# Performance work log

Hardware: AMD Instinct MI355X
Metric: run time of the kernel (lower is better)

The kernel has to match this reference:

```python
import jax, jax.numpy as jnp
import numpy as np

NEG_SLOPE = 0.2


def gat_layer(x, src, dst, W, att_src, att_dst, bias, concat):
    # x: [N, Fin]; W: [Fin, H*C]; att_*: [H, C]; bias: [H*C] or [C]
    n = x.shape[0]
    H, C = att_src.shape
    h = (x @ W).reshape(n, H, C)                      # [N,H,C]
    a_src = jnp.einsum('nhc,hc->nh', h, att_src)      # [N,H]
    a_dst = jnp.einsum('nhc,hc->nh', h, att_dst)      # [N,H]
    e = a_src[src] + a_dst[dst]                       # [E,H]
    e = jnp.where(e > 0, e, NEG_SLOPE * e)            # leaky_relu(0.2)
    # segment softmax over edges grouped by destination node
    m = jax.ops.segment_max(e, dst, num_segments=n)   # [N,H]
    m = jnp.where(jnp.isfinite(m), m, 0.0)            # empty segments
    ex = jnp.exp(e - m[dst])                          # [E,H]
    s = jax.ops.segment_sum(ex, dst, num_segments=n)  # [N,H]
    alpha = ex / (s[dst] + 1e-16)                     # [E,H]
    msg = h[src] * alpha[..., None]                   # [E,H,C]
    out = jax.ops.segment_sum(msg, dst, num_segments=n)  # [N,H,C]
    out = out.reshape(n, H * C) if concat else out.mean(axis=1)
    return out + bias


def setup_inputs() -> dict:
    key = jax.random.key(0)
    ks = jax.random.split(key, 10)
    N, E, FIN, HID, HEADS, OUT = 50000, 800000, 128, 64, 4, 16
    x = jax.random.normal(ks[0], (N, FIN), dtype=jnp.float32)
    edge_index = jax.random.randint(ks[1], (2, E), 0, N, dtype=jnp.int32)
    sc = 0.05
    return {
        'x': x,
        'edge_index': edge_index,
        'W1': jax.random.normal(ks[2], (FIN, HEADS * HID), jnp.float32) * sc,
        'att_src1': jax.random.normal(ks[3], (HEADS, HID), jnp.float32) * sc,
        'att_dst1': jax.random.normal(ks[4], (HEADS, HID), jnp.float32) * sc,
        'b1': jnp.zeros((HEADS * HID,), jnp.float32),
        'W2': jax.random.normal(ks[5], (HEADS * HID, OUT), jnp.float32) * sc,
        'att_src2': jax.random.normal(ks[6], (1, OUT), jnp.float32) * sc,
        'att_dst2': jax.random.normal(ks[7], (1, OUT), jnp.float32) * sc,
        'b2': jnp.zeros((OUT,), jnp.float32),
    }


def reference(x, edge_index, W1, att_src1, att_dst1, b1, W2, att_src2, att_dst2, b2):
    src, dst = edge_index[0], edge_index[1]
    h = gat_layer(x, src, dst, W1, att_src1, att_dst1, b1, concat=True)
    h = jax.nn.relu(h)
    # dropout is identity in eval mode
    out = gat_layer(h, src, dst, W2, att_src2, att_dst2, b2, concat=False)
    return out
```

## Files before the change

### kernel.cpp

```cpp
#include <hip/hip_runtime.h>
#include <hip/hip_bf16.h>

#define FIN 128
#define HC 256
#define H1 4
#define C1 64
#define OUT2 16

typedef __attribute__((ext_vector_type(8))) short bf16x8;
typedef __attribute__((ext_vector_type(4))) float f32x4;

__device__ inline float bf2f(unsigned short u) {
    union { unsigned int i; float f; } v; v.i = ((unsigned int)u) << 16; return v.f;
}
__device__ inline unsigned short f2bf(float f) {
    union { float f; unsigned int i; } v; v.f = f;
    unsigned int i = v.i;
    return (unsigned short)((i + 0x7FFFu + ((i >> 16) & 1u)) >> 16);
}
__device__ inline unsigned int pack2(float a, float b) {
    return (unsigned int)f2bf(a) | ((unsigned int)f2bf(b) << 16);
}

__global__ __launch_bounds__(256) void prep_kernel(
    const float* __restrict__ W1, unsigned short* __restrict__ W1t,
    const int* __restrict__ dst, int* __restrict__ counts, int E)
{
    int b = blockIdx.x;
    if (b < 128) {
        int t = b * 256 + threadIdx.x;
        int c = t >> 7, k = t & 127;
        W1t[t] = f2bf(W1[k * HC + c]);
    } else {
        int e = (b - 128) * 256 + threadIdx.x;
        if (e < E) atomicAdd(&counts[dst[e]], 1);
    }
}

__global__ __launch_bounds__(256) void gemm1_mfma_kernel(
    const float* __restrict__ x, const unsigned short* __restrict__ W1t,
    const float* __restrict__ att_src, const float* __restrict__ att_dst,
    unsigned short* __restrict__ h1, float* __restrict__ a_src,
    float* __restrict__ a_dst, int N)
{
    const int t  = threadIdx.x;
    const int wv = t >> 6;
    const int l  = t & 63;
    const int c0 = l & 15;
    const int h  = l >> 4;
    const int R0 = blockIdx.x * 64 + wv * 16;

    f32x4 acc[16];
    #pragma unroll
    for (int j = 0; j < 16; j++) acc[j] = (f32x4){0.f, 0.f, 0.f, 0.f};

    int arow = R0 + c0;
    if (arow > N - 1) arow = N - 1;
    const float* xrow = x + (size_t)arow * FIN;

    for (int kb = 0; kb < FIN; kb += 32) {
        float4 f0 = *(const float4*)&xrow[kb + 8 * h];
        float4 f1 = *(const float4*)&xrow[kb + 8 * h + 4];
        union { bf16x8 v; unsigned int u[4]; } af;
        af.u[0] = pack2(f0.x, f0.y);
        af.u[1] = pack2(f0.z, f0.w);
        af.u[2] = pack2(f1.x, f1.y);
        af.u[3] = pack2(f1.z, f1.w);
        #pragma unroll
        for (int j = 0; j < 16; j++) {
            int col = 16 * j + c0;
            union { bf16x8 v; uint4 u; } bf;
            bf.u = *(const uint4*)&W1t[(size_t)col * FIN + kb + 8 * h];
            acc[j] = __builtin_amdgcn_mfma_f32_16x16x32_bf16(af.v, bf.v, acc[j], 0, 0, 0);
        }
    }

    float avs[16], avd[16];
    #pragma unroll
    for (int j = 0; j < 16; j++) {
        avs[j] = att_src[16 * j + c0];
        avd[j] = att_dst[16 * j + c0];
    }
    f32x4 ps[4], pd[4];
    #pragma unroll
    for (int hd = 0; hd < 4; hd++) {
        ps[hd] = (f32x4){0.f, 0.f, 0.f, 0.f};
        pd[hd] = (f32x4){0.f, 0.f, 0.f, 0.f};
        #pragma unroll
        for (int jj = 0; jj < 4; jj++) {
            int j = 4 * hd + jj;
            #pragma unroll
            for (int r = 0; r < 4; r++) {
                ps[hd][r] = fmaf(acc[j][r], avs[j], ps[hd][r]);
                pd[hd][r] = fmaf(acc[j][r], avd[j], pd[hd][r]);
            }
        }
    }
    #pragma unroll
    for (int hd = 0; hd < 4; hd++)
        #pragma unroll
        for (int r = 0; r < 4; r++) {
            float s = ps[hd][r], d = pd[hd][r];
            s += __shfl_xor(s, 1, 64);  d += __shfl_xor(d, 1, 64);
            s += __shfl_xor(s, 2, 64);  d += __shfl_xor(d, 2, 64);
            s += __shfl_xor(s, 4, 64);  d += __shfl_xor(d, 4, 64);
            s += __shfl_xor(s, 8, 64);  d += __shfl_xor(d, 8, 64);
            ps[hd][r] = s;  pd[hd][r] = d;
        }
    {
        float s_sel = 0.f, d_sel = 0.f;
        #pragma unroll
        for (int hd = 0; hd < 4; hd++)
            #pragma unroll
            for (int r = 0; r < 4; r++) {
                bool m = (c0 == hd * 4 + r);
                s_sel = m ? ps[hd][r] : s_sel;
                d_sel = m ? pd[hd][r] : d_sel;
            }
        int row = R0 + 4 * h + (c0 & 3);
        if (row < N) {
            a_src[row * 4 + (c0 >> 2)] = s_sel;
            a_dst[row * 4 + (c0 >> 2)] = d_sel;
        }
    }

    #pragma unroll
    for (int r = 0; r < 4; r++) {
        int row = R0 + 4 * h + r;
        if (row < N) {
            unsigned short* hp = &h1[(size_t)row * HC + c0];
            #pragma unroll
            for (int j = 0; j < 16; j++)
                hp[16 * j] = f2bf(acc[j][r]);
        }
    }
}

__global__ __launch_bounds__(1024) void scan1_kernel(
    const int* __restrict__ counts, int* __restrict__ rowptr,
    int* __restrict__ bsum, int n)
{
    __shared__ int sm[1024];
    int tid = threadIdx.x;
    int i = blockIdx.x * 1024 + tid;
    int v = (i < n) ? counts[i] : 0;
    sm[tid] = v;
    __syncthreads();
    for (int off = 1; off < 1024; off <<= 1) {
        int tv = (tid >= off) ? sm[tid - off] : 0;
        __syncthreads();
        sm[tid] += tv;
        __syncthreads();
    }
    if (i < n) rowptr[i] = sm[tid] - v;
    if (tid == 1023) bsum[blockIdx.x] = sm[1023];
}

__global__ __launch_bounds__(1024) void scan2_kernel(
    int* __restrict__ bsum, int nb)
{
    __shared__ int sm[1024];
    int tid = threadIdx.x;
    int v = (tid < nb) ? bsum[tid] : 0;
    sm[tid] = v;
    __syncthreads();
    for (int off = 1; off < 1024; off <<= 1) {
        int tv = (tid >= off) ? sm[tid - off] : 0;
        __syncthreads();
        sm[tid] += tv;
        __syncthreads();
    }
    if (tid < nb) bsum[tid] = sm[tid] - v;
}

__global__ __launch_bounds__(256) void scatter_kernel(
    const int* __restrict__ src, const int* __restrict__ dst,
    const int* __restrict__ rowptr, const int* __restrict__ bsum,
    int* __restrict__ cursor,
    const float* __restrict__ a_src, const float* __restrict__ a_dst,
    uint4* __restrict__ csr_rec, int E)
{
    int e = blockIdx.x * blockDim.x + threadIdx.x;
    if (e >= E) return;
    int s = src[e], d = dst[e];
    int pos = rowptr[d] + bsum[d >> 10] + atomicAdd(&cursor[d], 1);
    float4 av = *(const float4*)&a_src[(size_t)s * 4];
    float4 bv = *(const float4*)&a_dst[(size_t)d * 4];
    float w0, w1, w2, w3, v;
    v = av.x + bv.x; v = v > 0.f ? v : 0.2f * v; w0 = __expf(v);
    v = av.y + bv.y; v = v > 0.f ? v : 0.2f * v; w1 = __expf(v);
    v = av.z + bv.z; v = v > 0.f ? v : 0.2f * v; w2 = __expf(v);
    v = av.w + bv.w; v = v > 0.f ? v : 0.2f * v; w3 = __expf(v);
    uint4 rec;
    rec.x = (unsigned int)s;
    rec.y = (unsigned int)d;
    rec.z = pack2(w0, w1);
    rec.w = pack2(w2, w3);
    csr_rec[pos] = rec;
}

__global__ __launch_bounds__(256) void agg1_kernel(
    const unsigned short* __restrict__ h1,
    const uint4* __restrict__ csr_rec, const int* __restrict__ rowptr,
    const int* __restrict__ bsum,
    const float* __restrict__ b1, const float* __restrict__ W2,
    const float* __restrict__ att_src2, const float* __restrict__ att_dst2,
    float* __restrict__ h2, float* __restrict__ a_src2, float* __restrict__ a_dst2,
    int N, int E)
{
    __shared__ float o_sh[4][272];
    int wave = (int)((blockIdx.x * blockDim.x + threadIdx.x) >> 6);
    if (wave >= N) return;
    int node = __builtin_amdgcn_readfirstlane(wave);
    int wv = (threadIdx.x >> 6);
    int l = threadIdx.x & 63;
    int h = l >> 4;
    int rs = rowptr[node] + bsum[node >> 10];
    int re = (node + 1 == N) ? E : rowptr[node + 1] + bsum[(node + 1) >> 10];
    float a0 = 0.f, a1 = 0.f, a2 = 0.f, a3 = 0.f, sw = 0.f;
    int p = rs;
    for (; p + 8 <= re; p += 8) {
        uint4 r[8];
        #pragma unroll
        for (int j = 0; j < 8; j++) r[j] = csr_rec[p + j];
        uint2 hv[8];
        #pragma unroll
        for (int j = 0; j < 8; j++)
            hv[j] = *(const uint2*)&h1[(size_t)(int)r[j].x * HC + 4 * l];
        #pragma unroll
        for (int j = 0; j < 8; j++) {
            unsigned int wsel = (h & 2) ? r[j].w : r[j].z;
            float wv_ = bf2f((unsigned short)((h & 1) ? (wsel >> 16) : (wsel & 0xffff)));
            a0 = fmaf(wv_, bf2f((unsigned short)(hv[j].x & 0xffff)), a0);
            a1 = fmaf(wv_, bf2f((unsigned short)(hv[j].x >> 16)), a1);
            a2 = fmaf(wv_, bf2f((unsigned short)(hv[j].y & 0xffff)), a2);
            a3 = fmaf(wv_, bf2f((unsigned short)(hv[j].y >> 16)), a3);
            sw += wv_;
        }
    }
    for (; p < re; p++) {
        uint4 r = csr_rec[p];
        uint2 hv = *(const uint2*)&h1[(size_t)(int)r.x * HC + 4 * l];
        unsigned int wsel = (h & 2) ? r.w : r.z;
        float wv_ = bf2f((unsigned short)((h & 1) ? (wsel >> 16) : (wsel & 0xffff)));
        a0 = fmaf(wv_, bf2f((unsigned short)(hv.x & 0xffff)), a0);
        a1 = fmaf(wv_, bf2f((unsigned short)(hv.x >> 16)), a1);
        a2 = fmaf(wv_, bf2f((unsigned short)(hv.y & 0xffff)), a2);
        a3 = fmaf(wv_, bf2f((unsigned short)(hv.y >> 16)), a3);
        sw += wv_;
    }
    float inv = 1.f / (sw + 1e-16f);
    float4 bv = *(const float4*)&b1[4 * l];
    float o0 = fmaxf(a0 * inv + bv.x, 0.f);
    float o1 = fmaxf(a1 * inv + bv.y, 0.f);
    float o2 = fmaxf(a2 * inv + bv.z, 0.f);
    float o3 = fmaxf(a3 * inv + bv.w, 0.f);

    float* my = o_sh[wv];
    *(float4*)&my[4 * l + 4 * h] = make_float4(o0, o1, o2, o3);
    asm volatile("s_waitcnt lgkmcnt(0)" ::: "memory");
    __builtin_amdgcn_sched_barrier(0);
    int q = h;
    int c = l & 15;
    float part = 0.f;
    #pragma unroll
    for (int m = 0; m < 16; m++) {
        float4 ov = *(const float4*)&my[68 * q + 4 * m];
        const float* w = &W2[(size_t)(64 * q + 4 * m) * OUT2 + c];
        part = fmaf(ov.x, w[0],  part);
        part = fmaf(ov.y, w[16], part);
        part = fmaf(ov.z, w[32], part);
        part = fmaf(ov.w, w[48], part);
    }
    part += __shfl_xor(part, 16, 64);
    part += __shfl_xor(part, 32, 64);
    float ps = part * att_src2[c];
    float pdv = part * att_dst2[c];
    ps += __shfl_xor(ps, 1, 64);  pdv += __shfl_xor(pdv, 1, 64);
    ps += __shfl_xor(ps, 2, 64);  pdv += __shfl_xor(pdv, 2, 64);
    ps += __shfl_xor(ps, 4, 64);  pdv += __shfl_xor(pdv, 4, 64);
    ps += __shfl_xor(ps, 8, 64);  pdv += __shfl_xor(pdv, 8, 64);
    if (l == 0) { a_src2[node] = ps; a_dst2[node] = pdv; }
    if (l < 16) h2[(size_t)node * OUT2 + l] = part;
}

__global__ __launch_bounds__(256) void agg2_kernel(
    const float* __restrict__ h2,
    const int* __restrict__ csr_rec_i,
    const float* __restrict__ a_src2, const float* __restrict__ a_dst2,
    const int* __restrict__ rowptr, const int* __restrict__ bsum,
    const float* __restrict__ b2, float* __restrict__ out, int N, int E)
{
    int wave = (int)((blockIdx.x * blockDim.x + threadIdx.x) >> 6);
    if (wave >= N) return;
    int node = __builtin_amdgcn_readfirstlane(wave);
    int l = threadIdx.x & 63;
    int g = l >> 4, c = l & 15;
    int rs = rowptr[node] + bsum[node >> 10];
    int re = (node + 1 == N) ? E : rowptr[node + 1] + bsum[(node + 1) >> 10];
    float ad = a_dst2[node];
    float acc = 0.f, sw = 0.f;
    int p = rs + g;
    for (; p + 12 < re; p += 16) {
        int sn0 = csr_rec_i[(size_t)(p     ) * 4];
        int sn1 = csr_rec_i[(size_t)(p +  4) * 4];
        int sn2 = csr_rec_i[(size_t)(p +  8) * 4];
        int sn3 = csr_rec_i[(size_t)(p + 12) * 4];
        float e0 = a_src2[sn0] + ad;
        float e1 = a_src2[sn1] + ad;
        float e2 = a_src2[sn2] + ad;
        float e3 = a_src2[sn3] + ad;
        float x0 = h2[(size_t)sn0 * OUT2 + c];
        float x1 = h2[(size_t)sn1 * OUT2 + c];
        float x2 = h2[(size_t)sn2 * OUT2 + c];
        float x3 = h2[(size_t)sn3 * OUT2 + c];
        e0 = e0 > 0.f ? e0 : 0.2f * e0;
        e1 = e1 > 0.f ? e1 : 0.2f * e1;
        e2 = e2 > 0.f ? e2 : 0.2f * e2;
        e3 = e3 > 0.f ? e3 : 0.2f * e3;
        float w0 = __expf(e0), w1 = __expf(e1), w2 = __expf(e2), w3 = __expf(e3);
        acc = fmaf(w0, x0, acc);
        acc = fmaf(w1, x1, acc);
        acc = fmaf(w2, x2, acc);
        acc = fmaf(w3, x3, acc);
        sw += (w0 + w1) + (w2 + w3);
    }
    for (; p < re; p += 4) {
        int sn = csr_rec_i[(size_t)p * 4];
        float e0 = a_src2[sn] + ad;
        e0 = e0 > 0.f ? e0 : 0.2f * e0;
        float w0 = __expf(e0);
        acc = fmaf(w0, h2[(size_t)sn * OUT2 + c], acc);
        sw += w0;
    }
    acc += __shfl_xor(acc, 16, 64);
    acc += __shfl_xor(acc, 32, 64);
    sw += __shfl_xor(sw, 16, 64);
    sw += __shfl_xor(sw, 32, 64);
    if (l < 16)
        out[(size_t)node * OUT2 + l] = acc / (sw + 1e-16f) + b2[l];
}

extern "C" void kernel_launch(void* const* d_in, const int* in_sizes, int n_in,
                              void* d_out, int out_size, void* d_ws, size_t ws_size,
                              hipStream_t stream)
{
    const float* x        = (const float*)d_in[0];
    const int*   ei       = (const int*)d_in[1];
    const float* W1       = (const float*)d_in[2];
    const float* att_src1 = (const float*)d_in[3];
    const float* att_dst1 = (const float*)d_in[4];
    const float* b1       = (const float*)d_in[5];
    const float* W2       = (const float*)d_in[6];
    const float* att_src2 = (const float*)d_in[7];
    const float* att_dst2 = (const float*)d_in[8];
    const float* b2       = (const float*)d_in[9];
    float* out = (float*)d_out;

    const int N = in_sizes[0] / FIN;
    const int E = in_sizes[1] / 2;
    const int* srcv = ei;
    const int* dstv = ei + E;

    char* base = (char*)d_ws;
    #define ALLOC(ptr, type, nelem) \
        type* ptr = (type*)base; base += (((size_t)(nelem) * sizeof(type) + 255) & ~(size_t)255);
    ALLOC(h1,      unsigned short, (size_t)N * HC)
    ALLOC(csr_rec, uint4,          (size_t)E)
    ALLOC(h2,      float,          (size_t)N * OUT2)
    ALLOC(a_src1v, float,          (size_t)N * 4)
    ALLOC(a_dst1v, float,          (size_t)N * 4)
    ALLOC(a_src2v, float,          (size_t)N)
    ALLOC(a_dst2v, float,          (size_t)N)
    ALLOC(counts,  int,            (size_t)2 * N)
    ALLOC(rowptr,  int,            (size_t)N + 1)
    ALLOC(bsum,    int,            1024)
    #undef ALLOC
    int* cursor = counts + N;
    unsigned short* W1t = (unsigned short*)csr_rec;

    const int nb = (N + 1023) / 1024;

    (void)hipMemsetAsync(counts, 0, sizeof(int) * 2 * (size_t)N, stream);

    prep_kernel<<<128 + (E + 255) / 256, 256, 0, stream>>>(W1, W1t, dstv, counts, E);
    gemm1_mfma_kernel<<<(N + 63) / 64, 256, 0, stream>>>(x, W1t, att_src1, att_dst1,
                                                         h1, a_src1v, a_dst1v, N);
    scan1_kernel<<<nb, 1024, 0, stream>>>(counts, rowptr, bsum, N);
    scan2_kernel<<<1, 1024, 0, stream>>>(bsum, nb);
    scatter_kernel<<<(E + 255) / 256, 256, 0, stream>>>(srcv, dstv, rowptr, bsum, cursor,
                                                        a_src1v, a_dst1v, csr_rec, E);
    agg1_kernel<<<(N + 3) / 4, 256, 0, stream>>>(h1, csr_rec, rowptr, bsum, b1, W2,
                                                 att_src2, att_dst2,
                                                 h2, a_src2v, a_dst2v, N, E);
    agg2_kernel<<<(N + 3) / 4, 256, 0, stream>>>(h2, (const int*)csr_rec,
                                                 a_src2v, a_dst2v, rowptr, bsum,
                                                 b2, out, N, E);
}
```

Measured before the change: 221.4 us.

## Store only source indices in CSR and recompute attention weights in aggregation

The scatter pass now writes a 4-byte source index per edge instead of a 16-byte record holding src, dst and packed bf16 attention weights. The layer-1 aggregation gathers a_src1 for each neighbour and recomputes leaky-relu and exp in place, and layer 2 reads the compact index array. This cuts scatter write traffic and CSR read traffic in both aggregation kernels, at the cost of an extra per-edge gather of a_src1 and redundant exp work across the 16 lanes of each head. The weights also stay in fp32 instead of being rounded to bf16.

```diff
diff --git a/kernel.cpp b/kernel.cpp
--- a/kernel.cpp
+++ b/kernel.cpp
@@ -176,33 +176,20 @@
 __global__ __launch_bounds__(256) void scatter_kernel(
     const int* __restrict__ src, const int* __restrict__ dst,
     const int* __restrict__ rowptr, const int* __restrict__ bsum,
-    int* __restrict__ cursor,
-    const float* __restrict__ a_src, const float* __restrict__ a_dst,
-    uint4* __restrict__ csr_rec, int E)
+    int* __restrict__ cursor, int* __restrict__ csr_src, int E)
 {
     int e = blockIdx.x * blockDim.x + threadIdx.x;
     if (e >= E) return;
-    int s = src[e], d = dst[e];
+    int d = dst[e];
     int pos = rowptr[d] + bsum[d >> 10] + atomicAdd(&cursor[d], 1);
-    float4 av = *(const float4*)&a_src[(size_t)s * 4];
-    float4 bv = *(const float4*)&a_dst[(size_t)d * 4];
-    float w0, w1, w2, w3, v;
-    v = av.x + bv.x; v = v > 0.f ? v : 0.2f * v; w0 = __expf(v);
-    v = av.y + bv.y; v = v > 0.f ? v : 0.2f * v; w1 = __expf(v);
-    v = av.z + bv.z; v = v > 0.f ? v : 0.2f * v; w2 = __expf(v);
-    v = av.w + bv.w; v = v > 0.f ? v : 0.2f * v; w3 = __expf(v);
-    uint4 rec;
-    rec.x = (unsigned int)s;
-    rec.y = (unsigned int)d;
-    rec.z = pack2(w0, w1);
-    rec.w = pack2(w2, w3);
-    csr_rec[pos] = rec;
+    csr_src[pos] = src[e];
 }
 
 __global__ __launch_bounds__(256) void agg1_kernel(
     const unsigned short* __restrict__ h1,
-    const uint4* __restrict__ csr_rec, const int* __restrict__ rowptr,
+    const int* __restrict__ csr_src, const int* __restrict__ rowptr,
     const int* __restrict__ bsum,
+    const float* __restrict__ a_src1, const float* __restrict__ a_dst1,
     const float* __restrict__ b1, const float* __restrict__ W2,
     const float* __restrict__ att_src2, const float* __restrict__ att_dst2,
     float* __restrict__ h2, float* __restrict__ a_src2, float* __restrict__ a_dst2,
@@ -217,20 +204,25 @@
     int h = l >> 4;
     int rs = rowptr[node] + bsum[node >> 10];
     int re = (node + 1 == N) ? E : rowptr[node + 1] + bsum[(node + 1) >> 10];
+    float ad = a_dst1[node * 4 + h];
     float a0 = 0.f, a1 = 0.f, a2 = 0.f, a3 = 0.f, sw = 0.f;
     int p = rs;
     for (; p + 8 <= re; p += 8) {
-        uint4 r[8];
-        #pragma unroll
-        for (int j = 0; j < 8; j++) r[j] = csr_rec[p + j];
+        int sn[8];
+        #pragma unroll
+        for (int j = 0; j < 8; j++) sn[j] = csr_src[p + j];
+        float asv[8];
         uint2 hv[8];
         #pragma unroll
-        for (int j = 0; j < 8; j++)
-            hv[j] = *(const uint2*)&h1[(size_t)(int)r[j].x * HC + 4 * l];
-        #pragma unroll
         for (int j = 0; j < 8; j++) {
-            unsigned int wsel = (h & 2) ? r[j].w : r[j].z;
-            float wv_ = bf2f((unsigned short)((h & 1) ? (wsel >> 16) : (wsel & 0xffff)));
+            asv[j] = a_src1[sn[j] * 4 + h];
+            hv[j] = *(const uint2*)&h1[(size_t)sn[j] * HC + 4 * l];
+        }
+        #pragma unroll
+        for (int j = 0; j < 8; j++) {
+            float e = asv[j] + ad;
+            e = e > 0.f ? e : 0.2f * e;
+            float wv_ = __expf(e);
             a0 = fmaf(wv_, bf2f((unsigned short)(hv[j].x & 0xffff)), a0);
             a1 = fmaf(wv_, bf2f((unsigned short)(hv[j].x >> 16)), a1);
             a2 = fmaf(wv_, bf2f((unsigned short)(hv[j].y & 0xffff)), a2);
@@ -239,10 +231,11 @@
         }
     }
     for (; p < re; p++) {
-        uint4 r = csr_rec[p];
-        uint2 hv = *(const uint2*)&h1[(size_t)(int)r.x * HC + 4 * l];
-        unsigned int wsel = (h & 2) ? r.w : r.z;
-        float wv_ = bf2f((unsigned short)((h & 1) ? (wsel >> 16) : (wsel & 0xffff)));
+        int sn = csr_src[p];
+        float e = a_src1[sn * 4 + h] + ad;
+        e = e > 0.f ? e : 0.2f * e;
+        float wv_ = __expf(e);
+        uint2 hv = *(const uint2*)&h1[(size_t)sn * HC + 4 * l];
         a0 = fmaf(wv_, bf2f((unsigned short)(hv.x & 0xffff)), a0);
         a1 = fmaf(wv_, bf2f((unsigned short)(hv.x >> 16)), a1);
         a2 = fmaf(wv_, bf2f((unsigned short)(hv.y & 0xffff)), a2);
@@ -286,7 +279,7 @@
 
 __global__ __launch_bounds__(256) void agg2_kernel(
     const float* __restrict__ h2,
-    const int* __restrict__ csr_rec_i,
+    const int* __restrict__ csr_src,
     const float* __restrict__ a_src2, const float* __restrict__ a_dst2,
     const int* __restrict__ rowptr, const int* __restrict__ bsum,
     const float* __restrict__ b2, float* __restrict__ out, int N, int E)
@@ -302,10 +295,10 @@
     float acc = 0.f, sw = 0.f;
     int p = rs + g;
     for (; p + 12 < re; p += 16) {
-        int sn0 = csr_rec_i[(size_t)(p     ) * 4];
-        int sn1 = csr_rec_i[(size_t)(p +  4) * 4];
-        int sn2 = csr_rec_i[(size_t)(p +  8) * 4];
-        int sn3 = csr_rec_i[(size_t)(p + 12) * 4];
+        int sn0 = csr_src[p];
+        int sn1 = csr_src[p + 4];
+        int sn2 = csr_src[p + 8];
+        int sn3 = csr_src[p + 12];
         float e0 = a_src2[sn0] + ad;
         float e1 = a_src2[sn1] + ad;
         float e2 = a_src2[sn2] + ad;
@@ -326,7 +319,7 @@
         sw += (w0 + w1) + (w2 + w3);
     }
     for (; p < re; p += 4) {
-        int sn = csr_rec_i[(size_t)p * 4];
+        int sn = csr_src[p];
         float e0 = a_src2[sn] + ad;
         e0 = e0 > 0.f ? e0 : 0.2f * e0;
         float w0 = __expf(e0);
@@ -366,7 +359,7 @@
     #define ALLOC(ptr, type, nelem) \
         type* ptr = (type*)base; base += (((size_t)(nelem) * sizeof(type) + 255) & ~(size_t)255);
     ALLOC(h1,      unsigned short, (size_t)N * HC)
-    ALLOC(csr_rec, uint4,          (size_t)E)
+    ALLOC(csr_src, int,            (size_t)E)
     ALLOC(h2,      float,          (size_t)N * OUT2)
     ALLOC(a_src1v, float,          (size_t)N * 4)
     ALLOC(a_dst1v, float,          (size_t)N * 4)
@@ -377,7 +370,7 @@
     ALLOC(bsum,    int,            1024)
     #undef ALLOC
     int* cursor = counts + N;
-    unsigned short* W1t = (unsigned short*)csr_rec;
+    unsigned short* W1t = (unsigned short*)csr_src;
 
     const int nb = (N + 1023) / 1024;
 
@@ -388,12 +381,13 @@
                                                          h1, a_src1v, a_dst1v, N);
     scan1_kernel<<<nb, 1024, 0, stream>>>(counts, rowptr, bsum, N);
     scan2_kernel<<<1, 1024, 0, stream>>>(bsum, nb);
-    scatter_kernel<<<(E + 255) / 256, 256, 0, stream>>>(srcv, dstv, rowptr, bsum, cursor,
-                                                        a_src1v, a_dst1v, csr_rec, E);
-    agg1_kernel<<<(N + 3) / 4, 256, 0, stream>>>(h1, csr_rec, rowptr, bsum, b1, W2,
+    scatter_kernel<<<(E + 255) / 256, 256, 0, stream>>>(srcv, dstv, rowptr, bsum,
+                                                        cursor, csr_src, E);
+    agg1_kernel<<<(N + 3) / 4, 256, 0, stream>>>(h1, csr_src, rowptr, bsum,
+                                                 a_src1v, a_dst1v, b1, W2,
                                                  att_src2, att_dst2,
                                                  h2, a_src2v, a_dst2v, N, E);
-    agg2_kernel<<<(N + 3) / 4, 256, 0, stream>>>(h2, (const int*)csr_rec,
+    agg2_kernel<<<(N + 3) / 4, 256, 0, stream>>>(h2, csr_src,
                                                  a_src2v, a_dst2v, rowptr, bsum,
                                                  b2, out, N, E);
 }
```

New measurement: 229.7 us. 3.7% more time.
